# Optimization experiments

Measured on AMD Instinct MI355X. Metric: run time of the kernel, lower is better.

## Reference

```python
import jax, jax.numpy as jnp
import numpy as np

NUM_CLASSES = 10
HIDDEN = 64
_LABEL2MASK_THRESHOL = 500


def setup_inputs() -> dict:
    key = jax.random.key(0)
    ks = jax.random.split(key, 5)
    B, h, w = 4, 60, 80
    feature1 = jax.random.normal(ks[0], (B, 512, h, w), jnp.float32)
    feature2 = jax.random.normal(ks[1], (B, 512, h // 2, w // 2), jnp.float32)
    # kaiming_normal (fan_in, relu): std = sqrt(2 / fan_in)
    w1 = jax.random.normal(ks[2], (HIDDEN, 512), jnp.float32) * np.sqrt(2.0 / 512)
    w2 = jax.random.normal(ks[3], (HIDDEN, 512), jnp.float32) * np.sqrt(2.0 / 512)
    wc = jax.random.normal(ks[4], (NUM_CLASSES + 1, HIDDEN), jnp.float32) * np.sqrt(2.0 / HIDDEN)
    b1 = jnp.zeros((HIDDEN,), jnp.float32)
    b2 = jnp.zeros((HIDDEN,), jnp.float32)
    bc = jnp.zeros((NUM_CLASSES + 1,), jnp.float32)
    return {"feature1": feature1, "feature2": feature2, "w1": w1, "b1": b1,
            "w2": w2, "b2": b2, "wc": wc, "bc": bc}


def _conv1x1(x, w, b):
    # x: (B,C,H,W), w: (O,C), b: (O,)
    return jnp.einsum('bchw,oc->bohw', x, w) + b[None, :, None, None]


def _resize2x(x, s):
    B, C, H, W = x.shape
    # torch nn.Upsample(mode='bilinear', align_corners=False) == half-pixel bilinear
    return jax.image.resize(x, (B, C, H * s, W * s), method='bilinear')


def _label2bbx(seg, num_classes, thresh):
    # seg: (B,H,W) int. Fixed-shape, fully vectorized version of the nested
    # python-loop bbox extraction. Rows with pixel count < thresh are -1.
    B, H, W = seg.shape
    cls = jnp.arange(1, num_classes, dtype=seg.dtype)        # skip background cls 0
    mask = seg[:, None, :, :] == cls[None, :, None, None]    # (B,K,H,W)
    cnt = mask.sum(axis=(2, 3))
    xs = jnp.arange(W, dtype=jnp.int32)[None, None, None, :]
    ys = jnp.arange(H, dtype=jnp.int32)[None, None, :, None]
    x1 = jnp.min(jnp.where(mask, xs, W), axis=(2, 3))
    x2 = jnp.max(jnp.where(mask, xs, -1), axis=(2, 3))
    y1 = jnp.min(jnp.where(mask, ys, H), axis=(2, 3))
    y2 = jnp.max(jnp.where(mask, ys, -1), axis=(2, 3))
    K = num_classes - 1
    bid = jnp.broadcast_to(jnp.arange(B, dtype=jnp.int32)[:, None], (B, K))
    cid = jnp.broadcast_to(cls.astype(jnp.int32)[None, :], (B, K))
    rows = jnp.stack([bid, x1.astype(jnp.int32), y1.astype(jnp.int32),
                      x2.astype(jnp.int32), y2.astype(jnp.int32), cid], axis=-1)  # (B,K,6)
    valid = (cnt >= thresh)[..., None]
    rows = jnp.where(valid, rows, -1)
    return rows.reshape(B * K, 6)


def reference(feature1, feature2, w1, b1, w2, b2, wc, bc):
    f1 = jax.nn.relu(_conv1x1(feature1, w1, b1))
    f2 = jax.nn.relu(_conv1x1(feature2, w2, b2))
    f2 = _resize2x(f2, 2)
    feat = _resize2x(f1 + f2, 8)              # (B,64,480,640)
    logits = _conv1x1(feat, wc, bc)           # (B,11,480,640)
    probability = jax.nn.softmax(logits, axis=1)
    segmentation = jnp.argmax(probability, axis=1)
    bbx = _label2bbx(segmentation, NUM_CLASSES, _LABEL2MASK_THRESHOL)
    return probability, segmentation, bbx
```

## Files before the change

kernel.cpp:

```cpp
#include <hip/hip_runtime.h>

#define BN 4
#define CIN 512
#define H1 60
#define W1 80
#define P1 4800
#define H2 30
#define W2 40
#define P2 1200
#define HID 64
#define NCLS 11
#define HF 480
#define WF 640
#define PF 307200
#define THRESH 500

#define WT1_OFF 0
#define WT2_OFF 32768
#define F2_OFF  65536
#define PART_OFF F2_OFF
#define L_OFF   (65536 + 307200)

__global__ void k0_init(const float* __restrict__ w1, const float* __restrict__ w2,
                        float* __restrict__ ws) {
    int idx = blockIdx.x * 256 + threadIdx.x;
    if (idx < 32768) {
        int c = idx >> 6, o = idx & 63;
        ws[WT1_OFF + idx] = w1[o * CIN + c];
    } else {
        int j = idx - 32768;
        int c = j >> 6, o = j & 63;
        ws[WT2_OFF + j] = w2[o * CIN + c];
    }
}

__global__ __launch_bounds__(384, 4) void k1_conv2(const float* __restrict__ x,
                                                   const float* __restrict__ b2,
                                                   float* __restrict__ ws) {
    __shared__ float part[4 * 48 * 65];
    const float* wt = ws + WT2_OFF;
    float* f2o = ws + F2_OFF;
    int blk = blockIdx.x;
    int b = blk / 25, tile = blk % 25;
    int t = threadIdx.x;
    int q = t % 12;
    int og = (t / 12) % 8;
    int ch = t / 96;
    int o0 = og * 8;
    int c0 = ch * 128;
    int p0 = tile * 48 + q * 4;

    float acc[4][8];
#pragma unroll
    for (int j = 0; j < 4; ++j)
#pragma unroll
        for (int i = 0; i < 8; ++i) acc[j][i] = 0.f;

    const float* xp = x + ((size_t)b * CIN + c0) * P2 + p0;
    const float* wp = wt + c0 * HID + o0;
#pragma unroll 4
    for (int c = 0; c < 128; ++c) {
        float4 xv = *(const float4*)(xp + (size_t)c * P2);
        float4 wa = *(const float4*)(wp + c * HID);
        float4 wb = *(const float4*)(wp + c * HID + 4);
        float w8[8] = {wa.x, wa.y, wa.z, wa.w, wb.x, wb.y, wb.z, wb.w};
        float x4[4] = {xv.x, xv.y, xv.z, xv.w};
#pragma unroll
        for (int j = 0; j < 4; ++j)
#pragma unroll
            for (int i = 0; i < 8; ++i) acc[j][i] = fmaf(w8[i], x4[j], acc[j][i]);
    }
#pragma unroll
    for (int j = 0; j < 4; ++j)
#pragma unroll
        for (int i = 0; i < 8; ++i)
            part[ch * 3120 + (q * 4 + j) * 65 + o0 + i] = acc[j][i];
    __syncthreads();

    int px = t >> 3;
    int oo = (t & 7) * 8;
    float v[8];
#pragma unroll
    for (int i = 0; i < 8; ++i) {
        int a = px * 65 + oo + i;
        float s = part[a] + part[3120 + a] + part[2 * 3120 + a] + part[3 * 3120 + a];
        v[i] = fmaxf(s + b2[oo + i], 0.f);
    }
    float* outp = f2o + ((size_t)b * P2 + tile * 48 + px) * HID + oo;
    *(float4*)outp = make_float4(v[0], v[1], v[2], v[3]);
    *(float4*)(outp + 4) = make_float4(v[4], v[5], v[6], v[7]);
}

__global__ __launch_bounds__(512, 4) void k2_conv1(const float* __restrict__ x,
                                                   const float* __restrict__ b1,
                                                   const float* __restrict__ wc,
                                                   const float* __restrict__ bc,
                                                   float* __restrict__ ws) {
    __shared__ float part[4 * 64 * 65];
    const float* wt = ws + WT1_OFF;
    const float* f2 = ws + F2_OFF;
    float* lout = ws + L_OFF;
    int blk = blockIdx.x;
    int b = blk / 75, tile = blk % 75;
    int t = threadIdx.x;
    int q = t & 15;
    int og = (t >> 4) & 7;
    int ch = t >> 7;
    int o0 = og * 8;
    int c0 = ch * 128;
    int p0 = tile * 64 + q * 4;

    float acc[4][8];
#pragma unroll
    for (int j = 0; j < 4; ++j)
#pragma unroll
        for (int i = 0; i < 8; ++i) acc[j][i] = 0.f;

    const float* xp = x + ((size_t)b * CIN + c0) * P1 + p0;
    const float* wp = wt + c0 * HID + o0;
#pragma unroll 4
    for (int c = 0; c < 128; ++c) {
        float4 xv = *(const float4*)(xp + (size_t)c * P1);
        float4 wa = *(const float4*)(wp + c * HID);
        float4 wb = *(const float4*)(wp + c * HID + 4);
        float w8[8] = {wa.x, wa.y, wa.z, wa.w, wb.x, wb.y, wb.z, wb.w};
        float x4[4] = {xv.x, xv.y, xv.z, xv.w};
#pragma unroll
        for (int j = 0; j < 4; ++j)
#pragma unroll
            for (int i = 0; i < 8; ++i) acc[j][i] = fmaf(w8[i], x4[j], acc[j][i]);
    }
#pragma unroll
    for (int j = 0; j < 4; ++j)
#pragma unroll
        for (int i = 0; i < 8; ++i)
            part[ch * 4160 + (q * 4 + j) * 65 + o0 + i] = acc[j][i];
    __syncthreads();

    {
        int px = t >> 3;
        int oo = (t & 7) * 8;
        int p = tile * 64 + px;
        int y = p / W1, xq = p - y * W1;
        float sy = fmaf((float)y, 0.5f, -0.25f);
        float fy = floorf(sy);
        float ty = sy - fy;
        int y0 = max(0, min(H2 - 1, (int)fy));
        int y1 = max(0, min(H2 - 1, (int)fy + 1));
        float sx = fmaf((float)xq, 0.5f, -0.25f);
        float fx = floorf(sx);
        float tx = sx - fx;
        int x0 = max(0, min(W2 - 1, (int)fx));
        int x1 = max(0, min(W2 - 1, (int)fx + 1));
        float wy0 = 1.f - ty, wx0 = 1.f - tx;
        const float* f2b = f2 + (size_t)b * P2 * HID;
        const float* r00 = f2b + (y0 * W2 + x0) * HID + oo;
        const float* r01 = f2b + (y0 * W2 + x1) * HID + oo;
        const float* r10 = f2b + (y1 * W2 + x0) * HID + oo;
        const float* r11 = f2b + (y1 * W2 + x1) * HID + oo;
#pragma unroll
        for (int i = 0; i < 8; ++i) {
            int a = px * 65 + oo + i;
            float s = part[a] + part[4160 + a] + part[2 * 4160 + a] + part[3 * 4160 + a];
            float f1v = fmaxf(s + b1[oo + i], 0.f);
            float v0 = r00[i] * wx0 + r01[i] * tx;
            float v1 = r10[i] * wx0 + r11[i] * tx;
            part[a] = f1v + (v0 * wy0 + v1 * ty);
        }
    }
    __syncthreads();

    {
        int px2 = t & 63;
        int kg = t >> 6;
        int k2i = (kg < 3) ? kg + 8 : 8;
        float l1 = bc[kg];
        float l2 = bc[k2i];
#pragma unroll 8
        for (int o = 0; o < HID; ++o) {
            float gv = part[px2 * 65 + o];
            l1 = fmaf(wc[kg * HID + o], gv, l1);
            l2 = fmaf(wc[k2i * HID + o], gv, l2);
        }
        float* lrow = lout + ((size_t)b * P1 + tile * 64 + px2) * 12;
        lrow[kg] = l1;
        if (kg < 3) lrow[kg + 8] = l2;
        else if (kg == 3) lrow[11] = 0.f;
    }
}

__global__ __launch_bounds__(256) void k4_main(float* __restrict__ out,
                                               float* __restrict__ ws) {
    __shared__ int s_cnt[9], s_x0[9], s_y0[9], s_x1[9], s_y1[9];
    const float* l = ws + L_OFF;
    int* partb = (int*)(ws + PART_OFF);
    int t = threadIdx.x;
    if (t < 9) { s_cnt[t] = 0; s_x0[t] = WF; s_y0[t] = HF; s_x1[t] = -1; s_y1[t] = -1; }
    __syncthreads();

    int fl = blockIdx.x * 256 + t;
    int b = fl / PF;
    int r = fl - b * PF;
    int Y = r / WF;
    int X = r - Y * WF;

    float sy = fmaf((float)Y, 0.125f, -0.4375f);
    float fy = floorf(sy);
    float ty = sy - fy;
    int y0 = max(0, min(H1 - 1, (int)fy));
    int y1 = max(0, min(H1 - 1, (int)fy + 1));
    float sx = fmaf((float)X, 0.125f, -0.4375f);
    float fx = floorf(sx);
    float tx = sx - fx;
    int x0 = max(0, min(W1 - 1, (int)fx));
    int x1 = max(0, min(W1 - 1, (int)fx + 1));
    float wy0 = 1.f - ty, wx0 = 1.f - tx;

    const float* lb = l + (size_t)b * P1 * 12;
    const float4* q00 = (const float4*)(lb + (y0 * W1 + x0) * 12);
    const float4* q01 = (const float4*)(lb + (y0 * W1 + x1) * 12);
    const float4* q10 = (const float4*)(lb + (y1 * W1 + x0) * 12);
    const float4* q11 = (const float4*)(lb + (y1 * W1 + x1) * 12);
    float l00[12], l01[12], l10[12], l11[12];
#pragma unroll
    for (int j = 0; j < 3; ++j) {
        ((float4*)l00)[j] = q00[j];
        ((float4*)l01)[j] = q01[j];
        ((float4*)l10)[j] = q10[j];
        ((float4*)l11)[j] = q11[j];
    }
    float li[11];
#pragma unroll
    for (int k = 0; k < 11; ++k) {
        float v0 = l00[k] * wx0 + l01[k] * tx;
        float v1 = l10[k] * wx0 + l11[k] * tx;
        li[k] = v0 * wy0 + v1 * ty;
    }
    int am = 0;
    float bm = li[0];
#pragma unroll
    for (int k = 1; k < 11; ++k) {
        if (li[k] > bm) { bm = li[k]; am = k; }
    }
    float e[11];
    float s = 0.f;
#pragma unroll
    for (int k = 0; k < 11; ++k) { e[k] = __expf(li[k] - bm); s += e[k]; }
    float rs = 1.f / s;
    size_t ob = (size_t)b * NCLS * PF + r;
#pragma unroll
    for (int k = 0; k < 11; ++k) out[ob + (size_t)k * PF] = e[k] * rs;
    out[(size_t)BN * NCLS * PF + fl] = (float)am;

    int lane = t & 63;
    int X0 = X & ~63;
    for (int c = 1; c <= 9; ++c) {
        unsigned long long m = __ballot(am == c);
        if (m != 0ULL && lane == 0) {
            int ci = c - 1;
            atomicAdd(&s_cnt[ci], (int)__popcll(m));
            atomicMin(&s_x0[ci], X0 + __builtin_ctzll(m));
            atomicMax(&s_x1[ci], X0 + 63 - __builtin_clzll(m));
            atomicMin(&s_y0[ci], Y);
            atomicMax(&s_y1[ci], Y);
        }
    }
    __syncthreads();
    if (t < 9) {
        int* pr = partb + blockIdx.x * 45 + t * 5;
        pr[0] = s_cnt[t];
        pr[1] = s_x0[t];
        pr[2] = s_y0[t];
        pr[3] = s_x1[t];
        pr[4] = s_y1[t];
    }
}

__global__ void k5_bbx(float* __restrict__ out, const float* __restrict__ ws) {
    const int* partb = (const int*)(ws + PART_OFF);
    int b = blockIdx.x / 9, c = blockIdx.x % 9;
    int t = threadIdx.x;
    int cnt = 0, mnx = WF, mny = HF, mxx = -1, mxy = -1;
    for (int i = t; i < 1200; i += 64) {
        const int* pr = partb + (size_t)(b * 1200 + i) * 45 + c * 5;
        cnt += pr[0];
        mnx = min(mnx, pr[1]);
        mny = min(mny, pr[2]);
        mxx = max(mxx, pr[3]);
        mxy = max(mxy, pr[4]);
    }
    for (int sft = 32; sft; sft >>= 1) {
        cnt += __shfl_xor(cnt, sft);
        mnx = min(mnx, __shfl_xor(mnx, sft));
        mny = min(mny, __shfl_xor(mny, sft));
        mxx = max(mxx, __shfl_xor(mxx, sft));
        mxy = max(mxy, __shfl_xor(mxy, sft));
    }
    if (t == 0) {
        float* row = out + (size_t)BN * NCLS * PF + (size_t)BN * PF + (size_t)(b * 9 + c) * 6;
        bool ok = cnt >= THRESH;
        row[0] = ok ? (float)b : -1.f;
        row[1] = ok ? (float)mnx : -1.f;
        row[2] = ok ? (float)mny : -1.f;
        row[3] = ok ? (float)mxx : -1.f;
        row[4] = ok ? (float)mxy : -1.f;
        row[5] = ok ? (float)(c + 1) : -1.f;
    }
}

extern "C" void kernel_launch(void* const* d_in, const int* in_sizes, int n_in,
                              void* d_out, int out_size, void* d_ws, size_t ws_size,
                              hipStream_t stream) {
    const float* f1 = (const float*)d_in[0];
    const float* f2 = (const float*)d_in[1];
    const float* w1 = (const float*)d_in[2];
    const float* b1 = (const float*)d_in[3];
    const float* w2 = (const float*)d_in[4];
    const float* b2 = (const float*)d_in[5];
    const float* wc = (const float*)d_in[6];
    const float* bc = (const float*)d_in[7];
    float* out = (float*)d_out;
    float* ws = (float*)d_ws;

    k0_init<<<dim3(256), dim3(256), 0, stream>>>(w1, w2, ws);
    k1_conv2<<<dim3(100), dim3(384), 0, stream>>>(f2, b2, ws);
    k2_conv1<<<dim3(300), dim3(512), 0, stream>>>(f1, b1, wc, bc, ws);
    k4_main<<<dim3(4800), dim3(256), 0, stream>>>(out, ws);
    k5_bbx<<<dim3(36), dim3(64), 0, stream>>>(out, ws);
}
```

Measured before the change: 200.3 us.

## Stage conv inputs into LDS via async global_load_lds with double buffering

Both 1x1 conv kernels now copy input tiles into LDS using global_load_lds DMA, double-buffered across channel chunks, instead of loading float4 directly from global memory per thread. Tiles are shrunk (16/32 pixels per block) and blocks reduced to 256 threads, giving 3x/2x more blocks for better CU coverage. The channel split is regrouped so each thread group reduces over interleaved channel chunks. The aim is to overlap memory latency with FMA work, at the cost of smaller tiles that reload weights more often and may have weaker global access coalescing.

```diff
diff --git a/kernel.cpp b/kernel.cpp
--- a/kernel.cpp
+++ b/kernel.cpp
@@ -21,6 +21,12 @@
 #define PART_OFF F2_OFF
 #define L_OFF   (65536 + 307200)
 
+__device__ __forceinline__ void dma16(const float* g, float* l) {
+    __builtin_amdgcn_global_load_lds(
+        (const __attribute__((address_space(1))) void*)g,
+        (__attribute__((address_space(3))) void*)l, 16, 0, 0);
+}
+
 __global__ void k0_init(const float* __restrict__ w1, const float* __restrict__ w2,
                         float* __restrict__ ws) {
     int idx = blockIdx.x * 256 + threadIdx.x;
@@ -34,21 +40,32 @@
     }
 }
 
-__global__ __launch_bounds__(384, 4) void k1_conv2(const float* __restrict__ x,
+__global__ __launch_bounds__(256, 4) void k1_conv2(const float* __restrict__ x,
                                                    const float* __restrict__ b2,
                                                    float* __restrict__ ws) {
-    __shared__ float part[4 * 48 * 65];
+    __shared__ float lds[8320];
     const float* wt = ws + WT2_OFF;
     float* f2o = ws + F2_OFF;
     int blk = blockIdx.x;
-    int b = blk / 25, tile = blk % 25;
+    int b = blk / 75, tile = blk % 75;
     int t = threadIdx.x;
-    int q = t % 12;
-    int og = (t / 12) % 8;
-    int ch = t / 96;
+    int l = t & 63, w = t >> 6;
+    int q = t & 3, og = (t >> 2) & 7, ch = t >> 5;
     int o0 = og * 8;
-    int c0 = ch * 128;
-    int p0 = tile * 48 + q * 4;
+    int p0 = tile * 16;
+    const float* xb = x + (size_t)b * CIN * P2 + p0;
+
+    auto stage = [&](int s) {
+        int buf = s & 1;
+#pragma unroll
+        for (int j = 0; j < 4; ++j) {
+            int r0 = j * 64 + w * 16;
+            int r  = r0 + (l >> 2);
+            int cg = (r >> 5) * 64 + s * 32 + (r & 31);
+            dma16(xb + (size_t)cg * P2 + (l & 3) * 4,
+                  lds + buf * 4096 + r0 * 16);
+        }
+    };
 
     float acc[4][8];
 #pragma unroll
@@ -56,59 +73,79 @@
 #pragma unroll
         for (int i = 0; i < 8; ++i) acc[j][i] = 0.f;
 
-    const float* xp = x + ((size_t)b * CIN + c0) * P2 + p0;
-    const float* wp = wt + c0 * HID + o0;
+    stage(0);
+    __syncthreads();
+    const float* wp = wt + (ch * 64) * HID + o0;
+    for (int s = 0; s < 2; ++s) {
+        if (s < 1) stage(s + 1);
+        const float* xs = lds + (s & 1) * 4096 + ch * 512 + q * 4;
 #pragma unroll 4
-    for (int c = 0; c < 128; ++c) {
-        float4 xv = *(const float4*)(xp + (size_t)c * P2);
-        float4 wa = *(const float4*)(wp + c * HID);
-        float4 wb = *(const float4*)(wp + c * HID + 4);
-        float w8[8] = {wa.x, wa.y, wa.z, wa.w, wb.x, wb.y, wb.z, wb.w};
-        float x4[4] = {xv.x, xv.y, xv.z, xv.w};
-#pragma unroll
-        for (int j = 0; j < 4; ++j)
-#pragma unroll
-            for (int i = 0; i < 8; ++i) acc[j][i] = fmaf(w8[i], x4[j], acc[j][i]);
+        for (int cc = 0; cc < 32; ++cc) {
+            float4 xv = *(const float4*)(xs + cc * 16);
+            const float* wr = wp + (s * 32 + cc) * HID;
+            float4 wa = *(const float4*)(wr);
+            float4 wb = *(const float4*)(wr + 4);
+            float w8[8] = {wa.x, wa.y, wa.z, wa.w, wb.x, wb.y, wb.z, wb.w};
+            float x4[4] = {xv.x, xv.y, xv.z, xv.w};
+#pragma unroll
+            for (int j = 0; j < 4; ++j)
+#pragma unroll
+                for (int i = 0; i < 8; ++i) acc[j][i] = fmaf(w8[i], x4[j], acc[j][i]);
+        }
+        __syncthreads();
     }
 #pragma unroll
     for (int j = 0; j < 4; ++j)
 #pragma unroll
         for (int i = 0; i < 8; ++i)
-            part[ch * 3120 + (q * 4 + j) * 65 + o0 + i] = acc[j][i];
-    __syncthreads();
-
-    int px = t >> 3;
-    int oo = (t & 7) * 8;
-    float v[8];
-#pragma unroll
-    for (int i = 0; i < 8; ++i) {
-        int a = px * 65 + oo + i;
-        float s = part[a] + part[3120 + a] + part[2 * 3120 + a] + part[3 * 3120 + a];
-        v[i] = fmaxf(s + b2[oo + i], 0.f);
-    }
-    float* outp = f2o + ((size_t)b * P2 + tile * 48 + px) * HID + oo;
-    *(float4*)outp = make_float4(v[0], v[1], v[2], v[3]);
-    *(float4*)(outp + 4) = make_float4(v[4], v[5], v[6], v[7]);
-}
-
-__global__ __launch_bounds__(512, 4) void k2_conv1(const float* __restrict__ x,
+            lds[ch * 1040 + (q * 4 + j) * 65 + o0 + i] = acc[j][i];
+    __syncthreads();
+
+    if (t < 128) {
+        int px = t >> 3, oo = (t & 7) * 8;
+        float v[8];
+#pragma unroll
+        for (int i = 0; i < 8; ++i) {
+            float s = 0.f;
+#pragma unroll
+            for (int c = 0; c < 8; ++c) s += lds[c * 1040 + px * 65 + oo + i];
+            v[i] = fmaxf(s + b2[oo + i], 0.f);
+        }
+        float* outp = f2o + ((size_t)b * P2 + p0 + px) * HID + oo;
+        *(float4*)outp = make_float4(v[0], v[1], v[2], v[3]);
+        *(float4*)(outp + 4) = make_float4(v[4], v[5], v[6], v[7]);
+    }
+}
+
+__global__ __launch_bounds__(256, 4) void k2_conv1(const float* __restrict__ x,
                                                    const float* __restrict__ b1,
                                                    const float* __restrict__ wc,
                                                    const float* __restrict__ bc,
                                                    float* __restrict__ ws) {
-    __shared__ float part[4 * 64 * 65];
+    __shared__ float lds[8320];
     const float* wt = ws + WT1_OFF;
     const float* f2 = ws + F2_OFF;
     float* lout = ws + L_OFF;
     int blk = blockIdx.x;
-    int b = blk / 75, tile = blk % 75;
+    int b = blk / 150, tile = blk % 150;
     int t = threadIdx.x;
-    int q = t & 15;
-    int og = (t >> 4) & 7;
-    int ch = t >> 7;
+    int l = t & 63, w = t >> 6;
+    int q = t & 7, og = (t >> 3) & 7, ch = t >> 6;
     int o0 = og * 8;
-    int c0 = ch * 128;
-    int p0 = tile * 64 + q * 4;
+    int p0 = tile * 32;
+    const float* xb = x + (size_t)b * CIN * P1 + p0;
+
+    auto stage = [&](int s) {
+        int buf = s & 1;
+#pragma unroll
+        for (int j = 0; j < 4; ++j) {
+            int r0 = j * 32 + w * 8;
+            int r  = r0 + (l >> 3);
+            int cg = (r >> 5) * 128 + s * 32 + (r & 31);
+            dma16(xb + (size_t)cg * P1 + (l & 7) * 4,
+                  lds + buf * 4096 + r0 * 32);
+        }
+    };
 
     float acc[4][8];
 #pragma unroll
@@ -116,31 +153,38 @@
 #pragma unroll
         for (int i = 0; i < 8; ++i) acc[j][i] = 0.f;
 
-    const float* xp = x + ((size_t)b * CIN + c0) * P1 + p0;
-    const float* wp = wt + c0 * HID + o0;
+    stage(0);
+    __syncthreads();
+    const float* wp = wt + (ch * 128) * HID + o0;
+    for (int s = 0; s < 4; ++s) {
+        if (s < 3) stage(s + 1);
+        const float* xs = lds + (s & 1) * 4096 + ch * 1024 + q * 4;
 #pragma unroll 4
-    for (int c = 0; c < 128; ++c) {
-        float4 xv = *(const float4*)(xp + (size_t)c * P1);
-        float4 wa = *(const float4*)(wp + c * HID);
-        float4 wb = *(const float4*)(wp + c * HID + 4);
-        float w8[8] = {wa.x, wa.y, wa.z, wa.w, wb.x, wb.y, wb.z, wb.w};
-        float x4[4] = {xv.x, xv.y, xv.z, xv.w};
-#pragma unroll
-        for (int j = 0; j < 4; ++j)
-#pragma unroll
-            for (int i = 0; i < 8; ++i) acc[j][i] = fmaf(w8[i], x4[j], acc[j][i]);
+        for (int cc = 0; cc < 32; ++cc) {
+            float4 xv = *(const float4*)(xs + cc * 32);
+            const float* wr = wp + (s * 32 + cc) * HID;
+            float4 wa = *(const float4*)(wr);
+            float4 wb = *(const float4*)(wr + 4);
+            float w8[8] = {wa.x, wa.y, wa.z, wa.w, wb.x, wb.y, wb.z, wb.w};
+            float x4[4] = {xv.x, xv.y, xv.z, xv.w};
+#pragma unroll
+            for (int j = 0; j < 4; ++j)
+#pragma unroll
+                for (int i = 0; i < 8; ++i) acc[j][i] = fmaf(w8[i], x4[j], acc[j][i]);
+        }
+        __syncthreads();
     }
 #pragma unroll
     for (int j = 0; j < 4; ++j)
 #pragma unroll
         for (int i = 0; i < 8; ++i)
-            part[ch * 4160 + (q * 4 + j) * 65 + o0 + i] = acc[j][i];
+            lds[ch * 2080 + (q * 4 + j) * 65 + o0 + i] = acc[j][i];
     __syncthreads();
 
     {
         int px = t >> 3;
         int oo = (t & 7) * 8;
-        int p = tile * 64 + px;
+        int p = p0 + px;
         int y = p / W1, xq = p - y * W1;
         float sy = fmaf((float)y, 0.5f, -0.25f);
         float fy = floorf(sy);
@@ -161,28 +205,28 @@
 #pragma unroll
         for (int i = 0; i < 8; ++i) {
             int a = px * 65 + oo + i;
-            float s = part[a] + part[4160 + a] + part[2 * 4160 + a] + part[3 * 4160 + a];
+            float s = lds[a] + lds[2080 + a] + lds[2 * 2080 + a] + lds[3 * 2080 + a];
             float f1v = fmaxf(s + b1[oo + i], 0.f);
             float v0 = r00[i] * wx0 + r01[i] * tx;
             float v1 = r10[i] * wx0 + r11[i] * tx;
-            part[a] = f1v + (v0 * wy0 + v1 * ty);
+            lds[a] = f1v + (v0 * wy0 + v1 * ty);
         }
     }
     __syncthreads();
 
     {
-        int px2 = t & 63;
-        int kg = t >> 6;
+        int px2 = t & 31;
+        int kg = t >> 5;
         int k2i = (kg < 3) ? kg + 8 : 8;
         float l1 = bc[kg];
         float l2 = bc[k2i];
 #pragma unroll 8
         for (int o = 0; o < HID; ++o) {
-            float gv = part[px2 * 65 + o];
+            float gv = lds[px2 * 65 + o];
             l1 = fmaf(wc[kg * HID + o], gv, l1);
             l2 = fmaf(wc[k2i * HID + o], gv, l2);
         }
-        float* lrow = lout + ((size_t)b * P1 + tile * 64 + px2) * 12;
+        float* lrow = lout + ((size_t)b * P1 + p0 + px2) * 12;
         lrow[kg] = l1;
         if (kg < 3) lrow[kg + 8] = l2;
         else if (kg == 3) lrow[11] = 0.f;
@@ -323,8 +367,8 @@
     float* ws = (float*)d_ws;
 
     k0_init<<<dim3(256), dim3(256), 0, stream>>>(w1, w2, ws);
-    k1_conv2<<<dim3(100), dim3(384), 0, stream>>>(f2, b2, ws);
-    k2_conv1<<<dim3(300), dim3(512), 0, stream>>>(f1, b1, wc, bc, ws);
+    k1_conv2<<<dim3(300), dim3(256), 0, stream>>>(f2, b2, ws);
+    k2_conv1<<<dim3(600), dim3(256), 0, stream>>>(f1, b1, wc, bc, ws);
     k4_main<<<dim3(4800), dim3(256), 0, stream>>>(out, ws);
     k5_bbx<<<dim3(36), dim3(64), 0, stream>>>(out, ws);
 }
```

Result: faster. 169.6 us (-15.4%).
